# Performance work log

Measured on AMD Instinct MI355X. Metric: run time of the kernel, lower is better.

Reference implementation:

```python
import jax, jax.numpy as jnp
import numpy as np

K_TOP = 8
TEMP = 1.0
GUMBEL_EPS = 1e-20
GEN_EPS = 1e-7
NEG_INF = -1e9


def _genconv(xn, src, dst, e, We, be, W1, b1, W2, b2):
    """GENConv: edge-proj, m=relu(x_src+e)+eps, per-dst softmax aggregation (t=1),
    residual add, then 2-layer MLP."""
    N = xn.shape[0]
    ep = e @ We + be                         # [E, C]
    m = jax.nn.relu(xn[src] + ep) + GEN_EPS  # [E, C]
    mx = jax.ops.segment_max(m, dst, num_segments=N)
    mx = jnp.where(jnp.isfinite(mx), mx, 0.0)
    w = jnp.exp(m - mx[dst])
    den = jax.ops.segment_sum(w, dst, num_segments=N)
    agg = jax.ops.segment_sum(w * m, dst, num_segments=N) / jnp.where(den > 0, den, 1.0)
    out = agg + xn
    return jax.nn.relu(out @ W1 + b1) @ W2 + b2


def setup_inputs() -> dict:
    key = jax.random.key(0)
    ks = jax.random.split(key, 16)
    N, E, D, ED = 1024, 16384, 128, 16
    H1, H2, OUT = 64, 64, 40
    s = 0.02
    return {
        "x": jax.random.normal(ks[0], (N, D), jnp.float32),
        "edge_attr": jax.random.normal(ks[1], (E, ED), jnp.float32),
        "gumbel_u": jax.random.uniform(ks[2], (N, N), jnp.float32),
        "mlp_w": jax.random.normal(ks[3], (ED + 2 * D, 1), jnp.float32) * s,
        "mlp_b": jnp.zeros((1,), jnp.float32),
        "c1_we": jax.random.normal(ks[4], (ED, D), jnp.float32) * s,
        "c1_be": jnp.zeros((D,), jnp.float32),
        "c1_w1": jax.random.normal(ks[5], (D, 2 * D), jnp.float32) * s,
        "c1_b1": jnp.zeros((2 * D,), jnp.float32),
        "c1_w2": jax.random.normal(ks[6], (2 * D, H1), jnp.float32) * s,
        "c1_b2": jnp.zeros((H1,), jnp.float32),
        "c2_we": jax.random.normal(ks[7], (ED, H1), jnp.float32) * s,
        "c2_be": jnp.zeros((H1,), jnp.float32),
        "c2_w1": jax.random.normal(ks[8], (H1, 2 * H1), jnp.float32) * s,
        "c2_b1": jnp.zeros((2 * H1,), jnp.float32),
        "c2_w2": jax.random.normal(ks[9], (2 * H1, H2), jnp.float32) * s,
        "c2_b2": jnp.zeros((H2,), jnp.float32),
        "fc_w": jax.random.normal(ks[10], (H2, OUT), jnp.float32) * s,
        "fc_b": jnp.zeros((OUT,), jnp.float32),
        "num_nodes": N,
        "edge_index": jax.random.randint(ks[11], (2, E), 0, N),
        "node_mask": jnp.ones((N,), jnp.int32),
    }


def reference(x, edge_attr, gumbel_u, mlp_w, mlp_b,
              c1_we, c1_be, c1_w1, c1_b1, c1_w2, c1_b2,
              c2_we, c2_be, c2_w1, c2_b1, c2_w2, c2_b2,
              fc_w, fc_b, num_nodes, edge_index, node_mask):
    N, D = x.shape
    src, dst = edge_index[0], edge_index[1]

    # dense adjacency (duplicate edges sum, only used as a zero/nonzero mask)
    adj = jnp.zeros((N, N), x.dtype).at[src, dst].add(1.0)

    # Edge-score MLP on concat([x_u, x_v*mask, edge_attr_dense]) decomposed
    # linearly (same math as scoring the dense [N,N,2D+ED] feature tensor).
    w_node, w_nb, w_e = mlp_w[:D], mlp_w[D:2 * D], mlp_w[2 * D:]
    s_edge = jnp.zeros((N, N), x.dtype).at[src, dst].set((edge_attr @ w_e)[:, 0])
    score = (x @ w_node) + (x @ w_nb).T * (adj > 0) + s_edge + mlp_b[0]
    score = jnp.where(adj == 0, NEG_INF, score)

    z = jax.nn.softmax(score, axis=-1)
    g = -jnp.log(-jnp.log(gumbel_u + GUMBEL_EPS) + GUMBEL_EPS)
    z = jax.nn.softmax((z + g) / TEMP, axis=-1)

    # top-k edge sampling; softmax output is strictly positive so valid_mask
    # (z>0) is always all-True and shapes stay static at N*k edges.
    _, topi = jax.lax.top_k(z, K_TOP)                       # [N, k]
    new_src = jnp.repeat(jnp.arange(N), K_TOP)
    new_dst = topi.reshape(-1)

    # match each new edge against old edge list (argmax of boolean equality,
    # unmatched edges fall back to index 0 exactly as torch argmax does)
    eq = (edge_index[0][None, :] == new_src[:, None]) & \
         (edge_index[1][None, :] == new_dst[:, None])       # [N*k, E]
    new_attr = edge_attr[jnp.argmax(eq, axis=-1)]

    h = _genconv(x, new_src, new_dst, new_attr, c1_we, c1_be, c1_w1, c1_b1, c1_w2, c1_b2)
    h = jax.nn.relu(h)
    h = _genconv(h, new_src, new_dst, new_attr, c2_we, c2_be, c2_w1, c2_b1, c2_w2, c2_b2)
    h = jax.nn.relu(h)
    out = h @ fc_w + fc_b
    # node_mask is all ones, so x[node_mask != 0] == identity; masked write
    # keeps static shapes under jit.
    return jnp.where((node_mask != 0)[:, None], out, 0.0)
```

## Files before the change

kernel.cpp:

```cpp
#include <hip/hip_runtime.h>
#include <cfloat>

#define NN   1024
#define NE   16384
#define D0   128
#define EDIM 16
#define NH1  64
#define NOUT 40
#define KTOP 8
#define NEGINF (-1000000000.0f)
#define MAXDEG 64

#define OFF_CNTS  0u
#define OFF_CNTD  4096u
#define OFF_SE    8192u
#define OFF_A     73728u
#define OFF_B     77824u
#define OFF_EM    81920u
#define OFF_SLOTS 114688u
#define OFF_SLOTD 376832u
#define OFF_H     638976u

__device__ __forceinline__ void amx(float& v, int& j, float ov, int oj) {
    if (ov > v || (ov == v && oj < j)) { v = ov; j = oj; }
}

__global__ __launch_bounds__(256) void prep_kernel(
    const float* __restrict__ x, const float* __restrict__ ea,
    const float* __restrict__ mlp_w, const int* __restrict__ ei,
    float* __restrict__ se, float* __restrict__ a, float* __restrict__ b,
    int* __restrict__ cnt_src, int* __restrict__ slot_src)
{
    const int bid = blockIdx.x, t = threadIdx.x;
    if (bid < 64) {
        int e = bid * 256 + t;
        float acc = 0.f;
        #pragma unroll
        for (int k = 0; k < EDIM; k++) acc += ea[e * EDIM + k] * mlp_w[2 * D0 + k];
        se[e] = acc;
        int s = ei[e];
        int p = atomicAdd(&cnt_src[s], 1);
        if (p < MAXDEG) slot_src[s * MAXDEG + p] = e;
    } else {
        int lane = t & 63, wid = t >> 6;
        int row = (bid - 64) * 4 + wid;
        const float* xr = x + row * D0;
        float x0 = xr[lane], x1 = xr[64 + lane];
        float sa = x0 * mlp_w[lane]       + x1 * mlp_w[64 + lane];
        float sb = x0 * mlp_w[128 + lane] + x1 * mlp_w[192 + lane];
        for (int s2 = 32; s2; s2 >>= 1) { sa += __shfl_down(sa, s2); sb += __shfl_down(sb, s2); }
        if (lane == 0) { a[row] = sa; b[row] = sb; }
    }
}

__global__ __launch_bounds__(256) void row_topk_kernel(
    const float* __restrict__ se, const float* __restrict__ mlp_b,
    const float* __restrict__ a, const float* __restrict__ b,
    const float* __restrict__ u, const int* __restrict__ ei,
    const int* __restrict__ cnt_src, const int* __restrict__ slot_src,
    int* __restrict__ em, int* __restrict__ cntd, int* __restrict__ slotd)
{
    __shared__ float sv[NN];
    __shared__ int   idmx[NN];
    __shared__ int   idmn[NN];
    __shared__ float wred[4];
    __shared__ int   wredj[4];
    __shared__ int   selj[KTOP];
    const int i = blockIdx.x, t = threadIdx.x;
    const int lane = t & 63, wid = t >> 6;
    const int rowoff = i * NN;
    const float bias = mlp_b[0];
    const float ai = a[i];

    #pragma unroll
    for (int q = 0; q < 4; q++) { int j = t + q * 256; idmx[j] = -1; idmn[j] = 0x7FFFFFFF; }
    __syncthreads();
    int deg = min(cnt_src[i], MAXDEG);
    if (t < deg) {
        int e = slot_src[i * MAXDEG + t];
        int dj = ei[NE + e];
        atomicMax(&idmx[dj], e);
        atomicMin(&idmn[dj], e);
    }
    __syncthreads();

    float lmax = NEGINF;
    #pragma unroll
    for (int q = 0; q < 4; q++) {
        int j = t + q * 256;
        int id = idmx[j];
        float s = (id >= 0) ? (((ai + b[j]) + se[id]) + bias) : NEGINF;
        sv[j] = s;
        lmax = fmaxf(lmax, s);
    }
    for (int s = 32; s; s >>= 1) lmax = fmaxf(lmax, __shfl_down(lmax, s));
    if (lane == 0) wred[wid] = lmax;
    __syncthreads();
    float rowmax = fmaxf(fmaxf(wred[0], wred[1]), fmaxf(wred[2], wred[3]));
    bool noedge = (rowmax == NEGINF);
    __syncthreads();

    float lsum = 0.f;
    #pragma unroll
    for (int q = 0; q < 4; q++) {
        int j = t + q * 256;
        float evv;
        if (noedge) evv = 1.0f;
        else { float s = sv[j]; evv = (s == NEGINF) ? 0.0f : expf(s - rowmax); }
        sv[j] = evv;
        lsum += evv;
    }
    for (int s = 32; s; s >>= 1) lsum += __shfl_down(lsum, s);
    if (lane == 0) wred[wid] = lsum;
    __syncthreads();
    float rsum = wred[0] + wred[1] + wred[2] + wred[3];
    __syncthreads();

    #pragma unroll
    for (int q = 0; q < 4; q++) {
        int j = t + q * 256;
        float z = sv[j] / rsum;
        float uu = u[rowoff + j];
        float g = -logf(-logf(uu + 1e-20f) + 1e-20f);
        sv[j] = z + g;
    }
    __syncthreads();

    for (int sel = 0; sel < KTOP; sel++) {
        float bv = -FLT_MAX; int bj = NN;
        #pragma unroll
        for (int q = 0; q < 4; q++) { int j = t + q * 256; amx(bv, bj, sv[j], j); }
        for (int s = 32; s; s >>= 1) {
            float ov = __shfl_down(bv, s); int oj = __shfl_down(bj, s);
            amx(bv, bj, ov, oj);
        }
        if (lane == 0) { wred[wid] = bv; wredj[wid] = bj; }
        __syncthreads();
        if (t == 0) {
            float v = wred[0]; int j = wredj[0];
            amx(v, j, wred[1], wredj[1]);
            amx(v, j, wred[2], wredj[2]);
            amx(v, j, wred[3], wredj[3]);
            selj[sel] = j;
            int mn = idmn[j];
            em[i * KTOP + sel] = (mn == 0x7FFFFFFF) ? 0 : mn;
            sv[j] = -FLT_MAX;
        }
        __syncthreads();
    }
    if (t < KTOP) {
        int j = selj[t];
        int n = i * KTOP + t;
        int p = atomicAdd(&cntd[j], 1);
        if (p < MAXDEG) slotd[j * MAXDEG + p] = n;
    }
}

__global__ __launch_bounds__(256) void genconv1_kernel(
    const float* __restrict__ x, const float* __restrict__ ea,
    const float* __restrict__ we_g, const float* __restrict__ be,
    const float* __restrict__ w1, const float* __restrict__ b1,
    const float* __restrict__ w2, const float* __restrict__ b2,
    const int* __restrict__ cntd, const int* __restrict__ slotd,
    const int* __restrict__ em, float* __restrict__ h)
{
    __shared__ int   slots[2][MAXDEG];
    __shared__ float eatt[2][MAXDEG * EDIM];
    __shared__ float arow[2][D0];
    __shared__ float t1s[2][2 * D0];
    const int t = threadIdx.x, sub = t >> 7, d = t & 127;
    const int r = blockIdx.x * 2 + sub;
    const int cnt = min(cntd[r], MAXDEG);
    if (d < cnt) slots[sub][d] = slotd[r * MAXDEG + d];
    __syncthreads();
    if (d == 0) {
        for (int p = 1; p < cnt; p++) {
            int v = slots[sub][p]; int q = p - 1;
            while (q >= 0 && slots[sub][q] > v) { slots[sub][q + 1] = slots[sub][q]; q--; }
            slots[sub][q + 1] = v;
        }
    }
    __syncthreads();
    for (int q = d; q < cnt * EDIM; q += 128)
        eatt[sub][q] = ea[em[slots[sub][q >> 4]] * EDIM + (q & 15)];
    __syncthreads();

    float wed[EDIM];
    #pragma unroll
    for (int k = 0; k < EDIM; k++) wed[k] = we_g[k * D0 + d];
    const float bed = be[d];

    float mxv = -FLT_MAX;
    for (int idx = 0; idx < cnt; idx++) {
        int src = slots[sub][idx] >> 3;
        float ep = bed;
        #pragma unroll
        for (int k = 0; k < EDIM; k++) ep += eatt[sub][idx * EDIM + k] * wed[k];
        float m = fmaxf(x[src * D0 + d] + ep, 0.f) + 1e-7f;
        mxv = fmaxf(mxv, m);
    }
    float den = 0.f, num = 0.f;
    for (int idx = 0; idx < cnt; idx++) {
        int src = slots[sub][idx] >> 3;
        float ep = bed;
        #pragma unroll
        for (int k = 0; k < EDIM; k++) ep += eatt[sub][idx * EDIM + k] * wed[k];
        float m = fmaxf(x[src * D0 + d] + ep, 0.f) + 1e-7f;
        float w = expf(m - mxv);
        den += w; num += w * m;
    }
    float agg = cnt ? num / (den > 0.f ? den : 1.f) : 0.f;
    arow[sub][d] = agg + x[r * D0 + d];
    __syncthreads();

    float acc0 = b1[d], acc1 = b1[d + D0];
    for (int k = 0; k < D0; k++) {
        float av = arow[sub][k];
        acc0 += av * w1[k * 2 * D0 + d];
        acc1 += av * w1[k * 2 * D0 + d + D0];
    }
    t1s[sub][d] = fmaxf(acc0, 0.f);
    t1s[sub][d + D0] = fmaxf(acc1, 0.f);
    __syncthreads();
    if (d < NH1) {
        float acc = b2[d];
        for (int k = 0; k < 2 * D0; k++) acc += t1s[sub][k] * w2[k * NH1 + d];
        h[r * NH1 + d] = fmaxf(acc, 0.f);
    }
}

__global__ __launch_bounds__(256) void genconv2_kernel(
    const float* __restrict__ h, const float* __restrict__ ea,
    const float* __restrict__ we_g, const float* __restrict__ be,
    const float* __restrict__ w1, const float* __restrict__ b1,
    const float* __restrict__ w2, const float* __restrict__ b2,
    const float* __restrict__ fcw, const float* __restrict__ fcb,
    const int* __restrict__ cntd, const int* __restrict__ slotd,
    const int* __restrict__ em, const int* __restrict__ mask,
    float* __restrict__ out)
{
    __shared__ int   slots[4][MAXDEG];
    __shared__ float eatt[4][MAXDEG * EDIM];
    __shared__ float arow[4][NH1];
    __shared__ float t2s[4][2 * NH1];
    __shared__ float h2s[4][NH1];
    const int t = threadIdx.x, sub = t >> 6, d = t & 63;
    const int r = blockIdx.x * 4 + sub;
    const int cnt = min(cntd[r], MAXDEG);
    if (d < cnt) slots[sub][d] = slotd[r * MAXDEG + d];
    __syncthreads();
    if (d == 0) {
        for (int p = 1; p < cnt; p++) {
            int v = slots[sub][p]; int q = p - 1;
            while (q >= 0 && slots[sub][q] > v) { slots[sub][q + 1] = slots[sub][q]; q--; }
            slots[sub][q + 1] = v;
        }
    }
    __syncthreads();
    for (int q = d; q < cnt * EDIM; q += 64)
        eatt[sub][q] = ea[em[slots[sub][q >> 4]] * EDIM + (q & 15)];
    __syncthreads();

    float wed[EDIM];
    #pragma unroll
    for (int k = 0; k < EDIM; k++) wed[k] = we_g[k * NH1 + d];
    const float bed = be[d];

    float mxv = -FLT_MAX;
    for (int idx = 0; idx < cnt; idx++) {
        int src = slots[sub][idx] >> 3;
        float ep = bed;
        #pragma unroll
        for (int k = 0; k < EDIM; k++) ep += eatt[sub][idx * EDIM + k] * wed[k];
        float m = fmaxf(h[src * NH1 + d] + ep, 0.f) + 1e-7f;
        mxv = fmaxf(mxv, m);
    }
    float den = 0.f, num = 0.f;
    for (int idx = 0; idx < cnt; idx++) {
        int src = slots[sub][idx] >> 3;
        float ep = bed;
        #pragma unroll
        for (int k = 0; k < EDIM; k++) ep += eatt[sub][idx * EDIM + k] * wed[k];
        float m = fmaxf(h[src * NH1 + d] + ep, 0.f) + 1e-7f;
        float w = expf(m - mxv);
        den += w; num += w * m;
    }
    float agg = cnt ? num / (den > 0.f ? den : 1.f) : 0.f;
    arow[sub][d] = agg + h[r * NH1 + d];
    __syncthreads();

    {
        float acc_a = b1[d], acc_b = b1[d + NH1];
        for (int k = 0; k < NH1; k++) {
            float av = arow[sub][k];
            acc_a += av * w1[k * 2 * NH1 + d];
            acc_b += av * w1[k * 2 * NH1 + d + NH1];
        }
        t2s[sub][d] = fmaxf(acc_a, 0.f);
        t2s[sub][d + NH1] = fmaxf(acc_b, 0.f);
    }
    __syncthreads();
    {
        float acc = b2[d];
        for (int k = 0; k < 2 * NH1; k++) acc += t2s[sub][k] * w2[k * NH1 + d];
        h2s[sub][d] = fmaxf(acc, 0.f);
    }
    __syncthreads();
    if (d < NOUT) {
        float acc = fcb[d];
        for (int k = 0; k < NH1; k++) acc += h2s[sub][k] * fcw[k * NOUT + d];
        out[r * NOUT + d] = (mask[r] != 0) ? acc : 0.f;
    }
}

extern "C" void kernel_launch(void* const* d_in, const int* in_sizes, int n_in,
                              void* d_out, int out_size, void* d_ws, size_t ws_size,
                              hipStream_t stream) {
    const float* x      = (const float*)d_in[0];
    const float* ea     = (const float*)d_in[1];
    const float* u      = (const float*)d_in[2];
    const float* mlp_w  = (const float*)d_in[3];
    const float* mlp_b  = (const float*)d_in[4];
    const float* c1_we  = (const float*)d_in[5];
    const float* c1_be  = (const float*)d_in[6];
    const float* c1_w1  = (const float*)d_in[7];
    const float* c1_b1  = (const float*)d_in[8];
    const float* c1_w2  = (const float*)d_in[9];
    const float* c1_b2  = (const float*)d_in[10];
    const float* c2_we  = (const float*)d_in[11];
    const float* c2_be  = (const float*)d_in[12];
    const float* c2_w1  = (const float*)d_in[13];
    const float* c2_b1  = (const float*)d_in[14];
    const float* c2_w2  = (const float*)d_in[15];
    const float* c2_b2  = (const float*)d_in[16];
    const float* fc_w   = (const float*)d_in[17];
    const float* fc_b   = (const float*)d_in[18];
    const int*   ei     = (const int*)d_in[20];
    const int*   mask   = (const int*)d_in[21];

    char* ws = (char*)d_ws;
    int*   cnt_src = (int*)(ws + OFF_CNTS);
    int*   cntd    = (int*)(ws + OFF_CNTD);
    float* se      = (float*)(ws + OFF_SE);
    float* a       = (float*)(ws + OFF_A);
    float* b       = (float*)(ws + OFF_B);
    int*   em      = (int*)(ws + OFF_EM);
    int*   slot_s  = (int*)(ws + OFF_SLOTS);
    int*   slotd   = (int*)(ws + OFF_SLOTD);
    float* h       = (float*)(ws + OFF_H);
    float* out     = (float*)d_out;

    hipMemsetAsync(ws + OFF_CNTS, 0, 8192, stream);
    prep_kernel<<<320, 256, 0, stream>>>(x, ea, mlp_w, ei, se, a, b, cnt_src, slot_s);
    row_topk_kernel<<<NN, 256, 0, stream>>>(se, mlp_b, a, b, u, ei, cnt_src, slot_s,
                                            em, cntd, slotd);
    genconv1_kernel<<<NN / 2, 256, 0, stream>>>(x, ea, c1_we, c1_be, c1_w1, c1_b1, c1_w2, c1_b2,
                                                cntd, slotd, em, h);
    genconv2_kernel<<<NN / 4, 256, 0, stream>>>(h, ea, c2_we, c2_be, c2_w1, c2_b1, c2_w2, c2_b2,
                                                fc_w, fc_b, cntd, slotd, em, mask, out);
}
```

Before: 157.8 us.

## Fuse prep and top-k into one wave-per-row kernel, drop memset and global bucketing

The memset, prep kernel and per-row top-k kernel are merged into one kernel. Each block handles four rows, and each block scans the full edge list itself to build per-row dst maps in shared memory. Scores are computed only for present edges, and the softmax, Gumbel and top-k steps run in registers with wave shuffles instead of block-wide syncs. The genconv kernels now rebuild their dst buckets by scanning the full nd array instead of reading global atomic slot lists. This removes two launches and the global atomics, at the cost of every block redundantly scanning all edges and all new edges.

```diff
diff --git a/kernel.cpp b/kernel.cpp
--- a/kernel.cpp
+++ b/kernel.cpp
@@ -10,149 +10,131 @@
 #define KTOP 8
 #define NEGINF (-1000000000.0f)
 #define MAXDEG 64
-
-#define OFF_CNTS  0u
-#define OFF_CNTD  4096u
-#define OFF_SE    8192u
-#define OFF_A     73728u
-#define OFF_B     77824u
-#define OFF_EM    81920u
-#define OFF_SLOTS 114688u
-#define OFF_SLOTD 376832u
-#define OFF_H     638976u
+#define PMAX   64
+
+#define OFF_EM  0u
+#define OFF_ND  32768u
+#define OFF_H   65536u
 
 __device__ __forceinline__ void amx(float& v, int& j, float ov, int oj) {
     if (ov > v || (ov == v && oj < j)) { v = ov; j = oj; }
 }
 
-__global__ __launch_bounds__(256) void prep_kernel(
+__global__ __launch_bounds__(256) void topk_kernel(
     const float* __restrict__ x, const float* __restrict__ ea,
-    const float* __restrict__ mlp_w, const int* __restrict__ ei,
-    float* __restrict__ se, float* __restrict__ a, float* __restrict__ b,
-    int* __restrict__ cnt_src, int* __restrict__ slot_src)
+    const float* __restrict__ u, const float* __restrict__ mlp_w,
+    const float* __restrict__ mlp_b, const int* __restrict__ ei,
+    int* __restrict__ nd, int* __restrict__ em)
 {
-    const int bid = blockIdx.x, t = threadIdx.x;
-    if (bid < 64) {
-        int e = bid * 256 + t;
-        float acc = 0.f;
-        #pragma unroll
-        for (int k = 0; k < EDIM; k++) acc += ea[e * EDIM + k] * mlp_w[2 * D0 + k];
-        se[e] = acc;
-        int s = ei[e];
-        int p = atomicAdd(&cnt_src[s], 1);
-        if (p < MAXDEG) slot_src[s * MAXDEG + p] = e;
-    } else {
-        int lane = t & 63, wid = t >> 6;
-        int row = (bid - 64) * 4 + wid;
-        const float* xr = x + row * D0;
-        float x0 = xr[lane], x1 = xr[64 + lane];
-        float sa = x0 * mlp_w[lane]       + x1 * mlp_w[64 + lane];
-        float sb = x0 * mlp_w[128 + lane] + x1 * mlp_w[192 + lane];
-        for (int s2 = 32; s2; s2 >>= 1) { sa += __shfl_down(sa, s2); sb += __shfl_down(sb, s2); }
-        if (lane == 0) { a[row] = sa; b[row] = sb; }
-    }
-}
-
-__global__ __launch_bounds__(256) void row_topk_kernel(
-    const float* __restrict__ se, const float* __restrict__ mlp_b,
-    const float* __restrict__ a, const float* __restrict__ b,
-    const float* __restrict__ u, const int* __restrict__ ei,
-    const int* __restrict__ cnt_src, const int* __restrict__ slot_src,
-    int* __restrict__ em, int* __restrict__ cntd, int* __restrict__ slotd)
-{
-    __shared__ float sv[NN];
-    __shared__ int   idmx[NN];
-    __shared__ int   idmn[NN];
-    __shared__ float wred[4];
-    __shared__ int   wredj[4];
-    __shared__ int   selj[KTOP];
-    const int i = blockIdx.x, t = threadIdx.x;
-    const int lane = t & 63, wid = t >> 6;
-    const int rowoff = i * NN;
-    const float bias = mlp_b[0];
-    const float ai = a[i];
-
-    #pragma unroll
-    for (int q = 0; q < 4; q++) { int j = t + q * 256; idmx[j] = -1; idmn[j] = 0x7FFFFFFF; }
-    __syncthreads();
-    int deg = min(cnt_src[i], MAXDEG);
-    if (t < deg) {
-        int e = slot_src[i * MAXDEG + t];
-        int dj = ei[NE + e];
-        atomicMax(&idmx[dj], e);
-        atomicMin(&idmn[dj], e);
-    }
-    __syncthreads();
-
-    float lmax = NEGINF;
-    #pragma unroll
-    for (int q = 0; q < 4; q++) {
-        int j = t + q * 256;
-        int id = idmx[j];
-        float s = (id >= 0) ? (((ai + b[j]) + se[id]) + bias) : NEGINF;
-        sv[j] = s;
-        lmax = fmaxf(lmax, s);
-    }
-    for (int s = 32; s; s >>= 1) lmax = fmaxf(lmax, __shfl_down(lmax, s));
-    if (lane == 0) wred[wid] = lmax;
-    __syncthreads();
-    float rowmax = fmaxf(fmaxf(wred[0], wred[1]), fmaxf(wred[2], wred[3]));
-    bool noedge = (rowmax == NEGINF);
-    __syncthreads();
-
-    float lsum = 0.f;
-    #pragma unroll
-    for (int q = 0; q < 4; q++) {
-        int j = t + q * 256;
-        float evv;
-        if (noedge) evv = 1.0f;
-        else { float s = sv[j]; evv = (s == NEGINF) ? 0.0f : expf(s - rowmax); }
-        sv[j] = evv;
-        lsum += evv;
-    }
-    for (int s = 32; s; s >>= 1) lsum += __shfl_down(lsum, s);
-    if (lane == 0) wred[wid] = lsum;
-    __syncthreads();
-    float rsum = wred[0] + wred[1] + wred[2] + wred[3];
-    __syncthreads();
-
-    #pragma unroll
-    for (int q = 0; q < 4; q++) {
-        int j = t + q * 256;
-        float z = sv[j] / rsum;
-        float uu = u[rowoff + j];
+    __shared__ int idmx[4 * NN];
+    __shared__ int idmn[4 * NN];
+    __shared__ int plj[4 * PMAX];
+    __shared__ int ple[4 * PMAX];
+    __shared__ int np[4];
+    const int t = threadIdx.x, lane = t & 63, w = t >> 6;
+    const int r0 = blockIdx.x * 4;
+
+    #pragma unroll
+    for (int q = 0; q < 16; q++) { idmx[t + q * 256] = -1; idmn[t + q * 256] = 0x7FFFFFFF; }
+    if (t < 4) np[t] = 0;
+    __syncthreads();
+
+    const int4* src4 = (const int4*)ei;
+    #pragma unroll
+    for (int q = 0; q < 16; q++) {
+        int idx4 = t + q * 256;
+        int4 v = src4[idx4];
+        int e0 = idx4 * 4;
+        #pragma unroll
+        for (int c = 0; c < 4; c++) {
+            int s = (c == 0) ? v.x : (c == 1) ? v.y : (c == 2) ? v.z : v.w;
+            unsigned rr = (unsigned)(s - r0);
+            if (rr < 4u) {
+                int e = e0 + c;
+                int d = ei[NE + e];
+                atomicMax(&idmx[rr * NN + d], e);
+                atomicMin(&idmn[rr * NN + d], e);
+            }
+        }
+    }
+    __syncthreads();
+
+    #pragma unroll
+    for (int q = 0; q < 16; q++) {
+        int idx = t + q * 256;
+        int e = idmx[idx];
+        if (e >= 0) {
+            int row = idx >> 10;
+            int p = atomicAdd(&np[row], 1);
+            if (p < PMAX) { plj[row * PMAX + p] = idx & 1023; ple[row * PMAX + p] = e; }
+        }
+    }
+    __syncthreads();
+
+    const int r = r0 + w;
+
+    float part = x[r * D0 + lane] * mlp_w[lane] + x[r * D0 + 64 + lane] * mlp_w[64 + lane];
+    for (int s2 = 32; s2; s2 >>= 1) part += __shfl_down(part, s2);
+    const float arb = __shfl(part, 0) + mlp_b[0];
+
+    float val[16];
+    #pragma unroll
+    for (int q = 0; q < 16; q++) val[q] = NEGINF;
+
+    const int npw = min(np[w], PMAX);
+    for (int p = 0; p < npw; p++) {
+        int j = plj[w * PMAX + p], e = ple[w * PMAX + p];
+        float pp = x[j * D0 + lane] * mlp_w[128 + lane]
+                 + x[j * D0 + 64 + lane] * mlp_w[192 + lane];
+        if (lane < 16) pp += ea[e * EDIM + lane] * mlp_w[256 + lane];
+        for (int s2 = 32; s2; s2 >>= 1) pp += __shfl_down(pp, s2);
+        float sc = __shfl(pp, 0) + arb;
+        #pragma unroll
+        for (int q = 0; q < 16; q++)
+            if (q == (j >> 6) && lane == (j & 63)) val[q] = sc;
+    }
+
+    float lm = NEGINF;
+    #pragma unroll
+    for (int q = 0; q < 16; q++) lm = fmaxf(lm, val[q]);
+    for (int s2 = 32; s2; s2 >>= 1) lm = fmaxf(lm, __shfl_down(lm, s2));
+    const float rowmax = __shfl(lm, 0);
+    const bool noedge = (rowmax == NEGINF);
+
+    float ls = 0.f;
+    #pragma unroll
+    for (int q = 0; q < 16; q++) {
+        float ev = noedge ? 1.0f : ((val[q] == NEGINF) ? 0.0f : expf(val[q] - rowmax));
+        val[q] = ev; ls += ev;
+    }
+    for (int s2 = 32; s2; s2 >>= 1) ls += __shfl_down(ls, s2);
+    const float rsum = __shfl(ls, 0);
+
+    const float* ur = u + r * NN;
+    #pragma unroll
+    for (int q = 0; q < 16; q++) {
+        float uu = ur[q * 64 + lane];
         float g = -logf(-logf(uu + 1e-20f) + 1e-20f);
-        sv[j] = z + g;
-    }
-    __syncthreads();
+        val[q] = val[q] / rsum + g;
+    }
 
     for (int sel = 0; sel < KTOP; sel++) {
         float bv = -FLT_MAX; int bj = NN;
         #pragma unroll
-        for (int q = 0; q < 4; q++) { int j = t + q * 256; amx(bv, bj, sv[j], j); }
-        for (int s = 32; s; s >>= 1) {
-            float ov = __shfl_down(bv, s); int oj = __shfl_down(bj, s);
+        for (int q = 0; q < 16; q++) amx(bv, bj, val[q], q * 64 + lane);
+        for (int s2 = 32; s2; s2 >>= 1) {
+            float ov = __shfl_down(bv, s2); int oj = __shfl_down(bj, s2);
             amx(bv, bj, ov, oj);
         }
-        if (lane == 0) { wred[wid] = bv; wredj[wid] = bj; }
-        __syncthreads();
-        if (t == 0) {
-            float v = wred[0]; int j = wredj[0];
-            amx(v, j, wred[1], wredj[1]);
-            amx(v, j, wred[2], wredj[2]);
-            amx(v, j, wred[3], wredj[3]);
-            selj[sel] = j;
-            int mn = idmn[j];
-            em[i * KTOP + sel] = (mn == 0x7FFFFFFF) ? 0 : mn;
-            sv[j] = -FLT_MAX;
-        }
-        __syncthreads();
-    }
-    if (t < KTOP) {
-        int j = selj[t];
-        int n = i * KTOP + t;
-        int p = atomicAdd(&cntd[j], 1);
-        if (p < MAXDEG) slotd[j * MAXDEG + p] = n;
+        int wj = __shfl(bj, 0);
+        if (lane == 0) {
+            int mn = idmn[w * NN + wj];
+            em[r * KTOP + sel] = (mn == 0x7FFFFFFF) ? 0 : mn;
+            nd[r * KTOP + sel] = wj;
+        }
+        #pragma unroll
+        for (int q = 0; q < 16; q++)
+            if (q == (wj >> 6) && lane == (wj & 63)) val[q] = -FLT_MAX;
     }
 }
 
@@ -161,18 +143,38 @@
     const float* __restrict__ we_g, const float* __restrict__ be,
     const float* __restrict__ w1, const float* __restrict__ b1,
     const float* __restrict__ w2, const float* __restrict__ b2,
-    const int* __restrict__ cntd, const int* __restrict__ slotd,
-    const int* __restrict__ em, float* __restrict__ h)
+    const int* __restrict__ nd, const int* __restrict__ em,
+    float* __restrict__ h)
 {
     __shared__ int   slots[2][MAXDEG];
     __shared__ float eatt[2][MAXDEG * EDIM];
     __shared__ float arow[2][D0];
     __shared__ float t1s[2][2 * D0];
+    __shared__ int   cnts[2];
     const int t = threadIdx.x, sub = t >> 7, d = t & 127;
-    const int r = blockIdx.x * 2 + sub;
-    const int cnt = min(cntd[r], MAXDEG);
-    if (d < cnt) slots[sub][d] = slotd[r * MAXDEG + d];
-    __syncthreads();
+    const int r0 = blockIdx.x * 2;
+    const int r = r0 + sub;
+    if (t < 2) cnts[t] = 0;
+    __syncthreads();
+
+    const int4* nd4 = (const int4*)nd;
+    #pragma unroll
+    for (int q = 0; q < 8; q++) {
+        int idx4 = t + q * 256;
+        int4 v = nd4[idx4];
+        int n0 = idx4 * 4;
+        #pragma unroll
+        for (int c = 0; c < 4; c++) {
+            int dj = (c == 0) ? v.x : (c == 1) ? v.y : (c == 2) ? v.z : v.w;
+            unsigned rr = (unsigned)(dj - r0);
+            if (rr < 2u) {
+                int p = atomicAdd(&cnts[rr], 1);
+                if (p < MAXDEG) slots[rr][p] = n0 + c;
+            }
+        }
+    }
+    __syncthreads();
+    const int cnt = min(cnts[sub], MAXDEG);
     if (d == 0) {
         for (int p = 1; p < cnt; p++) {
             int v = slots[sub][p]; int q = p - 1;
@@ -235,20 +237,39 @@
     const float* __restrict__ w1, const float* __restrict__ b1,
     const float* __restrict__ w2, const float* __restrict__ b2,
     const float* __restrict__ fcw, const float* __restrict__ fcb,
-    const int* __restrict__ cntd, const int* __restrict__ slotd,
-    const int* __restrict__ em, const int* __restrict__ mask,
-    float* __restrict__ out)
+    const int* __restrict__ nd, const int* __restrict__ em,
+    const int* __restrict__ mask, float* __restrict__ out)
 {
     __shared__ int   slots[4][MAXDEG];
     __shared__ float eatt[4][MAXDEG * EDIM];
     __shared__ float arow[4][NH1];
     __shared__ float t2s[4][2 * NH1];
     __shared__ float h2s[4][NH1];
+    __shared__ int   cnts[4];
     const int t = threadIdx.x, sub = t >> 6, d = t & 63;
-    const int r = blockIdx.x * 4 + sub;
-    const int cnt = min(cntd[r], MAXDEG);
-    if (d < cnt) slots[sub][d] = slotd[r * MAXDEG + d];
-    __syncthreads();
+    const int r0 = blockIdx.x * 4;
+    const int r = r0 + sub;
+    if (t < 4) cnts[t] = 0;
+    __syncthreads();
+
+    const int4* nd4 = (const int4*)nd;
+    #pragma unroll
+    for (int q = 0; q < 8; q++) {
+        int idx4 = t + q * 256;
+        int4 v = nd4[idx4];
+        int n0 = idx4 * 4;
+        #pragma unroll
+        for (int c = 0; c < 4; c++) {
+            int dj = (c == 0) ? v.x : (c == 1) ? v.y : (c == 2) ? v.z : v.w;
+            unsigned rr = (unsigned)(dj - r0);
+            if (rr < 4u) {
+                int p = atomicAdd(&cnts[rr], 1);
+                if (p < MAXDEG) slots[rr][p] = n0 + c;
+            }
+        }
+    }
+    __syncthreads();
+    const int cnt = min(cnts[sub], MAXDEG);
     if (d == 0) {
         for (int p = 1; p < cnt; p++) {
             int v = slots[sub][p]; int q = p - 1;
@@ -339,23 +360,14 @@
     const int*   mask   = (const int*)d_in[21];
 
     char* ws = (char*)d_ws;
-    int*   cnt_src = (int*)(ws + OFF_CNTS);
-    int*   cntd    = (int*)(ws + OFF_CNTD);
-    float* se      = (float*)(ws + OFF_SE);
-    float* a       = (float*)(ws + OFF_A);
-    float* b       = (float*)(ws + OFF_B);
-    int*   em      = (int*)(ws + OFF_EM);
-    int*   slot_s  = (int*)(ws + OFF_SLOTS);
-    int*   slotd   = (int*)(ws + OFF_SLOTD);
-    float* h       = (float*)(ws + OFF_H);
-    float* out     = (float*)d_out;
-
-    hipMemsetAsync(ws + OFF_CNTS, 0, 8192, stream);
-    prep_kernel<<<320, 256, 0, stream>>>(x, ea, mlp_w, ei, se, a, b, cnt_src, slot_s);
-    row_topk_kernel<<<NN, 256, 0, stream>>>(se, mlp_b, a, b, u, ei, cnt_src, slot_s,
-                                            em, cntd, slotd);
+    int*   em = (int*)(ws + OFF_EM);
+    int*   nd = (int*)(ws + OFF_ND);
+    float* h  = (float*)(ws + OFF_H);
+    float* out = (float*)d_out;
+
+    topk_kernel<<<NN / 4, 256, 0, stream>>>(x, ea, u, mlp_w, mlp_b, ei, nd, em);
     genconv1_kernel<<<NN / 2, 256, 0, stream>>>(x, ea, c1_we, c1_be, c1_w1, c1_b1, c1_w2, c1_b2,
-                                                cntd, slotd, em, h);
+                                                nd, em, h);
     genconv2_kernel<<<NN / 4, 256, 0, stream>>>(h, ea, c2_we, c2_be, c2_w1, c2_b1, c2_w2, c2_b2,
-                                                fc_w, fc_b, cntd, slotd, em, mask, out);
-}
+                                                fc_w, fc_b, nd, em, mask, out);
+}
```

New measurement: 180.4 us. 14.3% more time.
